# Kernel tuning notes

Hardware: AMD Instinct MI355X
Metric: run time of the kernel (lower is better)

The kernel has to match this reference:

```python
import jax, jax.numpy as jnp
import numpy as np

HID, EMB, VOCAB, NLAYERS = 512, 256, 64, 2
BS, SLEN, LLEN = 64, 128, 1024


def _p(key, shape, scale):
    return jax.random.normal(key, shape, dtype=jnp.float32) * scale


def setup_inputs() -> dict:
    key = jax.random.key(0)
    ks = jax.random.split(key, 24)
    s_h = 1.0 / np.sqrt(HID)
    inp = {
        "y": jax.random.randint(ks[0], (BS, SLEN), 0, VOCAB, dtype=jnp.int64),
        "encoder_h": jax.random.normal(ks[1], (BS, LLEN, HID), dtype=jnp.float32),
        # embedding table
        "emb": _p(ks[2], (VOCAB, EMB), 1.0),
        # attention LSTMCell: input = hidden + embedding
        "att_Wih": _p(ks[3], (4 * HID, HID + EMB), s_h),
        "att_Whh": _p(ks[4], (4 * HID, HID), s_h),
        "att_bih": _p(ks[5], (4 * HID,), s_h),
        "att_bhh": _p(ks[6], (4 * HID,), s_h),
        # stacked LSTMCells (NLAYERS, ...)
        "rnn_Wih": _p(ks[7], (NLAYERS, 4 * HID, HID), s_h),
        "rnn_Whh": _p(ks[8], (NLAYERS, 4 * HID, HID), s_h),
        "rnn_bih": _p(ks[9], (NLAYERS, 4 * HID), s_h),
        "rnn_bhh": _p(ks[10], (NLAYERS, 4 * HID), s_h),
        # AttentionContext mlp_s / mlp_h
        "Ws_w": _p(ks[11], (HID, HID), s_h),
        "Ws_b": _p(ks[12], (HID,), s_h),
        "Wh_w": _p(ks[13], (HID, HID), s_h),
        "Wh_b": _p(ks[14], (HID,), s_h),
        # output MLP: Linear(2H -> H), ReLU, Linear(H -> V)
        "W1": _p(ks[15], (HID, 2 * HID), 1.0 / np.sqrt(2 * HID)),
        "b1": _p(ks[16], (HID,), s_h),
        "W2": _p(ks[17], (VOCAB, HID), s_h),
        "b2": _p(ks[18], (VOCAB,), s_h),
    }
    return inp


def _lstm_cell(x, h, c, Wih, Whh, bih, bhh):
    gates = x @ Wih.T + bih + h @ Whh.T + bhh  # (B, 4H)
    i, f, g, o = jnp.split(gates, 4, axis=-1)
    c2 = jax.nn.sigmoid(f) * c + jax.nn.sigmoid(i) * jnp.tanh(g)
    h2 = jax.nn.sigmoid(o) * jnp.tanh(c2)
    return h2, c2


def reference(y, encoder_h, emb, att_Wih, att_Whh, att_bih, att_bhh,
              rnn_Wih, rnn_Whh, rnn_bih, rnn_bhh,
              Ws_w, Ws_b, Wh_w, Wh_b, W1, b1, W2, b2):
    B, S = y.shape
    H = att_Whh.shape[1]
    nl = rnn_Wih.shape[0]
    y_emb = emb[y]  # (B, S, E)
    # mlp_h(encoder_h) is loop-invariant; hoist it (same math as per-step recompute)
    h_e = encoder_h @ Wh_w.T + Wh_b  # (B, L, H)

    def step(carry, x_t):
        h0, c0, hs, cs, att = carry
        rnn_in = jnp.concatenate([x_t, att], axis=-1)  # (B, E+H)
        h0, c0 = _lstm_cell(rnn_in, h0, c0, att_Wih, att_Whh, att_bih, att_bhh)
        prev = h0
        new_h, new_c = [], []
        for l in range(nl):
            hl, cl = _lstm_cell(prev, hs[l], cs[l], rnn_Wih[l], rnn_Whh[l],
                                rnn_bih[l], rnn_bhh[l])
            new_h.append(hl)
            new_c.append(cl)
            prev = hl
        hs2 = jnp.stack(new_h)
        cs2 = jnp.stack(new_c)
        # attention on h_t[-1]
        s_e = prev @ Ws_w.T + Ws_b  # (B, H)
        e = jnp.einsum('bh,blh->bl', s_e, h_e)
        a = jax.nn.softmax(e, axis=-1)
        ctx = jnp.einsum('bl,blh->bh', a, h_e)  # (B, H)
        mlp_in = jnp.concatenate([prev, ctx], axis=-1)  # (B, 2H)
        logits = jax.nn.relu(mlp_in @ W1.T + b1) @ W2.T + b2  # (B, V)
        return (h0, c0, hs2, cs2, ctx), logits

    z = jnp.zeros((B, H), dtype=encoder_h.dtype)
    zz = jnp.zeros((nl, B, H), dtype=encoder_h.dtype)
    init = (z, z, zz, zz, z)
    _, y_out = jax.lax.scan(step, init, jnp.swapaxes(y_emb, 0, 1))  # (S, B, V)
    y_out = jnp.swapaxes(y_out, 0, 1)  # (B, S, V)
    return y_out.reshape(B * S, -1)
```

## Files before the change

### kernel.cpp

```cpp
#include <hip/hip_runtime.h>
#include <hip/hip_fp16.h>

#define HID   512
#define EMB   256
#define VOCAB 64
#define BS    64
#define SLEN  128
#define LLEN  1024
#define G4    2048
#define NB    256
#define NT    512
#define ASTR  66
#define ASZ   (128 * ASTR)

typedef unsigned u32x4 __attribute__((ext_vector_type(4)));

__device__ __forceinline__ u32x4 vldq(const unsigned* p) {
    return *reinterpret_cast<const volatile u32x4*>(p);
}
__device__ __forceinline__ float vld1(const float* p) {
    return *reinterpret_cast<const volatile float*>(p);
}
__device__ __forceinline__ void vst1(float* p, float v) {
    *reinterpret_cast<volatile float*>(p) = v;
}
__device__ __forceinline__ void vstu(unsigned* p, unsigned v) {
    *reinterpret_cast<volatile unsigned*>(p) = v;
}
__device__ __forceinline__ unsigned packh2(float x, float y) {
    __half2 h = __floats2half2_rn(x, y);
    return *reinterpret_cast<unsigned*>(&h);
}

struct SCell { float As[2 * ASZ]; float red[8][10][66]; };
struct SAttn { float u_s[512]; float w_s[32]; float msh[4];
               float accs[16][34]; unsigned enc[32 * 261]; };
struct SLog  { float red[16 * 33]; };
union SMem { SCell c; SAttn a; SLog lg; };

__device__ __forceinline__ void gridbar(unsigned* bar, unsigned nb)
{
    __syncthreads();
    const int t = threadIdx.x;
    if (t < 64) {
        if (t == 0)
            __hip_atomic_store(bar + blockIdx.x, nb, __ATOMIC_RELAXED,
                               __HIP_MEMORY_SCOPE_AGENT);
        for (;;) {
            bool ok = true;
#pragma unroll
            for (int i = 0; i < 4; ++i) {
                unsigned v = __hip_atomic_load(bar + i * 64 + t, __ATOMIC_RELAXED,
                                               __HIP_MEMORY_SCOPE_AGENT);
                ok &= (v >= nb);
            }
            if (__all((int)ok)) break;
            __builtin_amdgcn_s_sleep(1);
        }
    }
    __syncthreads();
}

__global__ __launch_bounds__(256)
void k_embed16T(const int* __restrict__ y, const float* __restrict__ emb,
                __half* __restrict__ xemb16)
{
    int i = blockIdx.x * 256 + threadIdx.x;
    int b  = i & 63;
    int e  = (i >> 6) & 255;
    int ts = i >> 14;
    xemb16[i] = __float2half(emb[y[b * SLEN + ts] * EMB + e]);
}

__global__ __launch_bounds__(256)
void k_cast(const float* __restrict__ src, __half* __restrict__ dst, int n4)
{
    int i = blockIdx.x * 256 + threadIdx.x;
    int stride = gridDim.x * 256;
    for (; i < n4; i += stride) {
        float4 v = reinterpret_cast<const float4*>(src)[i];
        reinterpret_cast<__half2*>(dst)[2 * i]     = __floats2half2_rn(v.x, v.y);
        reinterpret_cast<__half2*>(dst)[2 * i + 1] = __floats2half2_rn(v.z, v.w);
    }
}

__global__ __launch_bounds__(256)
void k_pmat(const float* __restrict__ Whw, const float* __restrict__ Wsw,
            const float* __restrict__ Wsb, float* __restrict__ P,
            float* __restrict__ p0)
{
    const int i = blockIdx.x;
    const int t = threadIdx.x;
    float a0 = 0.f, a1 = 0.f, ap = 0.f;
    for (int h = 0; h < HID; ++h) {
        float whi = Whw[h * HID + i];
        a0 += whi * Wsw[h * HID + t];
        a1 += whi * Wsw[h * HID + t + 256];
        ap += whi * Wsb[h];
    }
    P[i * HID + t]       = a0;
    P[i * HID + t + 256] = a1;
    if (t == 0) p0[i] = ap;
}

__global__ __launch_bounds__(256)
void k_fold(const float* __restrict__ aWih, const float* __restrict__ W1,
            const float* __restrict__ Whw, const float* __restrict__ Whb,
            const float* __restrict__ abih, const float* __restrict__ b1,
            float* __restrict__ Wp, float* __restrict__ W1bp,
            float* __restrict__ bihEff, float* __restrict__ b1eff)
{
    const int r = blockIdx.x;
    const int t = threadIdx.x;
    __shared__ float ssrc[512];
    const float* src;
    float* dst;
    if (r < G4) { src = aWih + (size_t)r * (EMB + HID) + EMB; dst = Wp + (size_t)r * HID; }
    else        { src = W1 + (size_t)(r - G4) * (2 * HID) + HID; dst = W1bp + (size_t)(r - G4) * HID; }
    ssrc[t]       = src[t];
    ssrc[t + 256] = src[t + 256];
    __syncthreads();
    float a0 = 0.f, a1 = 0.f;
    for (int h = 0; h < HID; ++h) {
        const float s = ssrc[h];
        a0 += s * Whw[h * HID + t];
        a1 += s * Whw[h * HID + t + 256];
    }
    dst[t]       = a0;
    dst[t + 256] = a1;
    if (t == 0) {
        float bb = 0.f;
        for (int h = 0; h < HID; ++h) bb += ssrc[h] * Whb[h];
        if (r < G4) bihEff[r] = abih[r] + bb;
        else        b1eff[r - G4] = b1[r - G4] + bb;
    }
}

template<int NTILES, int NR, bool VOL>
__device__ __forceinline__ void segScanT(float* As, const __half* A,
    const float* const* w, float* acc, int wv, int lane)
{
    const int t = threadIdx.x;
    const unsigned* ga = reinterpret_cast<const unsigned*>(A) + (size_t)t * 8;
    const int kRow = t >> 2;
    const int c0   = (t & 3) * 16;
    u32x4 Ra[2], Rb[2];

#define LOADT(R, j) do { const unsigned* _p = ga + (size_t)(j) * 4096;            \
        if (VOL) { R[0] = vldq(_p); R[1] = vldq(_p + 4); }                        \
        else { R[0] = *reinterpret_cast<const u32x4*>(_p);                        \
               R[1] = *reinterpret_cast<const u32x4*>(_p + 4); } } while (0)

    LOADT(Ra, 0);
    __syncthreads();
#pragma unroll
    for (int j = 0; j < NTILES; ++j) {
        float2* dst = reinterpret_cast<float2*>(As + (j & 1) * ASZ + kRow * ASTR + c0);
        const u32x4* R = (j & 1) ? Rb : Ra;
#pragma unroll
        for (int q = 0; q < 2; ++q)
#pragma unroll
            for (int h = 0; h < 4; ++h) {
                unsigned uw = R[q][h];
                dst[q * 4 + h] = __half22float2(*reinterpret_cast<const __half2*>(&uw));
            }
        if (j + 1 < NTILES) { if (j & 1) { LOADT(Ra, j + 1); } else { LOADT(Rb, j + 1); } }
        __syncthreads();
        const float* as = As + (j & 1) * ASZ + (wv * 16) * ASTR + lane;
#pragma unroll
        for (int kk = 0; kk < 16; ++kk) {
            const float a = as[kk * ASTR];
            const int k = j * 128 + wv * 16 + kk;
#pragma unroll
            for (int r = 0; r < NR; ++r)
                acc[r] += a * w[r][k];
        }
    }
#undef LOADT
}

__device__ __forceinline__ void packRows(__half* dstH, int i0, const float (&htmp)[2][64])
{
    const int t = threadIdx.x;
    if (t < 64) {
        const int hl = t >> 5;
        const int b2 = (t & 31) * 2;
        vstu(reinterpret_cast<unsigned*>(dstH) + (size_t)(i0 + hl) * 32 + (t & 31),
             packh2(htmp[hl][b2], htmp[hl][b2 + 1]));
    }
}

__device__ __forceinline__ void phaseA(SMem& sm, int i0,
    const __half* xT, const __half* chatT, const __half* h0rT,
    const float* __restrict__ aWih, const float* __restrict__ Wp,
    const float* __restrict__ aWhh, const float* __restrict__ W1bp,
    const float* __restrict__ bihEff, const float* __restrict__ abhh,
    float* cp, const float* hpartPriv, __half* h0wT, float* hid,
    float (&htmp)[2][64], int wv, int lane)
{
    float acc[10] = {};
    {
        const float* w8[8];
#pragma unroll
        for (int r = 0; r < 8; ++r)
            w8[r] = aWih + (size_t)((r >> 1) * HID + i0 + (r & 1)) * (EMB + HID);
        segScanT<2, 8, false>(sm.c.As, xT, w8, acc, wv, lane);
    }
    {
        const float* w10[10];
#pragma unroll
        for (int r = 0; r < 8; ++r)
            w10[r] = Wp + (size_t)((r >> 1) * HID + i0 + (r & 1)) * HID;
        w10[8] = W1bp + (size_t)i0 * HID;
        w10[9] = W1bp + (size_t)(i0 + 1) * HID;
        segScanT<4, 10, true>(sm.c.As, chatT, w10, acc, wv, lane);
    }
    {
        const float* w8[8];
#pragma unroll
        for (int r = 0; r < 8; ++r)
            w8[r] = aWhh + (size_t)((r >> 1) * HID + i0 + (r & 1)) * HID;
        segScanT<4, 8, true>(sm.c.As, h0rT, w8, acc, wv, lane);
    }
#pragma unroll
    for (int r = 0; r < 10; ++r) sm.c.red[wv][r][lane] = acc[r];
    __syncthreads();
    const int t = threadIdx.x;
    if (t < 128) {
        const int b = t & 63, hl = t >> 6;
        float gs[4];
#pragma unroll
        for (int g = 0; g < 4; ++g) {
            const int row = g * HID + i0 + hl;
            float s = bihEff[row] + abhh[row];
#pragma unroll
            for (int w = 0; w < 8; ++w) s += sm.c.red[w][g * 2 + hl][b];
            gs[g] = s;
        }
        const float ig = 1.f / (1.f + __expf(-gs[0]));
        const float fg = 1.f / (1.f + __expf(-gs[1]));
        const float gg = tanhf(gs[2]);
        const float og = 1.f / (1.f + __expf(-gs[3]));
        const float c2 = fg * cp[hl * 64 + b] + ig * gg;
        cp[hl * 64 + b] = c2;
        htmp[hl][b] = og * tanhf(c2);
    } else if (t < 256) {
        const int b = t & 63, hl = (t >> 6) - 2;
        float s = hpartPriv[hl * 64 + b];
#pragma unroll
        for (int w = 0; w < 8; ++w) s += sm.c.red[w][8 + hl][b];
        vst1(hid + (size_t)b * HID + i0 + hl, fmaxf(s, 0.f));
    }
    __syncthreads();
    packRows(h0wT, i0, htmp);
}

__device__ __forceinline__ void phaseR(SMem& sm, int i0,
    const __half* inT, const __half* recT,
    const float* __restrict__ Wih, const float* __restrict__ Whh,
    const float* __restrict__ bih, const float* __restrict__ bhh,
    float* cp, __half* hOutT, float (&htmp)[2][64], int wv, int lane)
{
    float acc[8] = {};
    {
        const float* w8[8];
#pragma unroll
        for (int r = 0; r < 8; ++r)
            w8[r] = Wih + (size_t)((r >> 1) * HID + i0 + (r & 1)) * HID;
        segScanT<4, 8, true>(sm.c.As, inT, w8, acc, wv, lane);
    }
    {
        const float* w8[8];
#pragma unroll
        for (int r = 0; r < 8; ++r)
            w8[r] = Whh + (size_t)((r >> 1) * HID + i0 + (r & 1)) * HID;
        segScanT<4, 8, true>(sm.c.As, recT, w8, acc, wv, lane);
    }
#pragma unroll
    for (int r = 0; r < 8; ++r) sm.c.red[wv][r][lane] = acc[r];
    __syncthreads();
    const int t = threadIdx.x;
    if (t < 128) {
        const int b = t & 63, hl = t >> 6;
        float gs[4];
#pragma unroll
        for (int g = 0; g < 4; ++g) {
            const int row = g * HID + i0 + hl;
            float s = bih[row] + bhh[row];
#pragma unroll
            for (int w = 0; w < 8; ++w) s += sm.c.red[w][g * 2 + hl][b];
            gs[g] = s;
        }
        const float ig = 1.f / (1.f + __expf(-gs[0]));
        const float fg = 1.f / (1.f + __expf(-gs[1]));
        const float gg = tanhf(gs[2]);
        const float og = 1.f / (1.f + __expf(-gs[3]));
        const float c2 = fg * cp[hl * 64 + b] + ig * gg;
        cp[hl * 64 + b] = c2;
        htmp[hl][b] = og * tanhf(c2);
    }
    __syncthreads();
    packRows(hOutT, i0, htmp);
}

__device__ __forceinline__ void logitsPhase(SMem& sm, int bid,
    const float* hid, const float* __restrict__ W2,
    const float* __restrict__ b2, float* __restrict__ out, int tstep)
{
    const int t  = threadIdx.x;
    const int b  = bid & 63;
    const int vg = bid >> 6;
    const int vp = t >> 5;
    const int kk = t & 31;
    float hreg[16];
    const float* hp = hid + (size_t)b * HID + kk * 16;
#pragma unroll
    for (int k = 0; k < 16; ++k) hreg[k] = vld1(hp + k);
    const float* w = W2 + (size_t)(vg * 16 + vp) * HID + kk * 16;
    float s = 0.f;
#pragma unroll
    for (int k = 0; k < 16; ++k) s += hreg[k] * w[k];
    __syncthreads();
    sm.lg.red[vp * 33 + kk] = s;
    __syncthreads();
    if (t < 16) {
        float acc = b2[vg * 16 + t];
#pragma unroll
        for (int k = 0; k < 32; ++k) acc += sm.lg.red[t * 33 + k];
        out[((size_t)b * SLEN + tstep) * VOCAB + vg * 16 + t] = acc;
    }
}

__device__ __forceinline__ void phaseD(SMem& sm, int i0,
    const __half* prevT, const float* __restrict__ Pm,
    const float* __restrict__ p0v, const float* __restrict__ W1,
    const float* __restrict__ b1eff, float* u, float* hpartPriv,
    int wv, int lane)
{
    float acc[4] = {};
    const float* w4[4];
    w4[0] = Pm + (size_t)i0 * HID;
    w4[1] = Pm + (size_t)(i0 + 1) * HID;
    w4[2] = W1 + (size_t)i0 * (2 * HID);
    w4[3] = W1 + (size_t)(i0 + 1) * (2 * HID);
    segScanT<4, 4, true>(sm.c.As, prevT, w4, acc, wv, lane);
#pragma unroll
    for (int r = 0; r < 4; ++r) sm.c.red[wv][r][lane] = acc[r];
    __syncthreads();
    const int t = threadIdx.x;
    if (t < 256) {
        const int b = t & 63, r = t >> 6;
        float s = 0.f;
#pragma unroll
        for (int w = 0; w < 8; ++w) s += sm.c.red[w][r][b];
        if (r < 2) vst1(u + (size_t)b * HID + i0 + r, s + p0v[i0 + r]);
        else       hpartPriv[(r - 2) * 64 + b] = s + b1eff[i0 + r - 2];
    }
}

__device__ __forceinline__ void phaseE(SMem& sm, int bid,
    const float* u, const __half* __restrict__ enc16,
    float* pm, float* ps, float* pv)
{
    const int t    = threadIdx.x;
    const int b    = bid >> 2;
    const int ch   = bid & 3;
    const int half = t >> 8;
    const int col  = t & 255;
    const int le   = t & 31;
    const int seg  = t >> 5;
    const int sq   = t & 15;
    const int sl   = (t >> 4) & 31;

    sm.a.u_s[t] = vld1(u + (size_t)b * HID + t);
    if (t == 0) { sm.a.msh[0] = -3.0e38f; sm.a.msh[1] = 0.f; sm.a.msh[2] = 0.f; }
    float vx = 0.f, vy = 0.f;

    const uint4* src = reinterpret_cast<const uint4*>(enc16 + ((size_t)b * LLEN + ch * 256) * HID);
    uint4 R[4];
#pragma unroll
    for (int p = 0; p < 4; ++p) R[p] = src[(size_t)sl * 64 + p * 16 + sq];
    __syncthreads();

    for (int blk = 0; blk < 8; ++blk) {
        {
            unsigned* dst = &sm.a.enc[sl * 261];
#pragma unroll
            for (int p = 0; p < 4; ++p) {
                const int c4 = (p * 16 + sq) * 4;
                dst[c4] = R[p].x; dst[c4+1] = R[p].y; dst[c4+2] = R[p].z; dst[c4+3] = R[p].w;
            }
        }
        __syncthreads();
        if (blk < 7) {
#pragma unroll
            for (int p = 0; p < 4; ++p)
                R[p] = src[((size_t)(blk + 1) * 32 + sl) * 64 + p * 16 + sq];
        }
        {
            float eacc = 0.f;
            const unsigned* er = &sm.a.enc[le * 261];
            const float* us = sm.a.u_s;
#pragma unroll
            for (int uu = 0; uu < 16; ++uu) {
                const int uo = seg * 16 + uu;
                unsigned uw = er[uo];
                float2 f2 = __half22float2(*reinterpret_cast<const __half2*>(&uw));
                eacc += us[2 * uo] * f2.x + us[2 * uo + 1] * f2.y;
            }
            sm.a.accs[seg][le] = eacc;
        }
        __syncthreads();
        if (t < 32) {
            float e = 0.f;
#pragma unroll
            for (int s2 = 0; s2 < 16; ++s2) e += sm.a.accs[s2][t];
            float bm = e;
#pragma unroll
            for (int off = 16; off > 0; off >>= 1) bm = fmaxf(bm, __shfl_xor(bm, off));
            const float m_old = sm.a.msh[0];
            const float m_new = fmaxf(m_old, bm);
            const float wl = __expf(e - m_new);
            float sw = wl;
#pragma unroll
            for (int off = 16; off > 0; off >>= 1) sw += __shfl_xor(sw, off);
            sm.a.w_s[t] = wl;
            if (t == 0) {
                const float sc = __expf(m_old - m_new);
                sm.a.msh[2] = sc;
                sm.a.msh[1] = sm.a.msh[1] * sc + sw;
                sm.a.msh[0] = m_new;
            }
        }
        __syncthreads();
        {
            const float sc = sm.a.msh[2];
            vx *= sc; vy *= sc;
#pragma unroll
            for (int ll = 0; ll < 16; ++ll) {
                const int l = half * 16 + ll;
                const float wl = sm.a.w_s[l];
                unsigned uw = sm.a.enc[l * 261 + col];
                float2 f2 = __half22float2(*reinterpret_cast<const __half2*>(&uw));
                vx += wl * f2.x; vy += wl * f2.y;
            }
        }
        __syncthreads();
    }
    if (half == 1) { sm.a.u_s[2 * col] = vx; sm.a.u_s[2 * col + 1] = vy; }
    __syncthreads();
    if (half == 0) {
        vx += sm.a.u_s[2 * col];
        vy += sm.a.u_s[2 * col + 1];
        const int pc = b * 4 + ch;
        vst1(pv + (size_t)pc * HID + 2 * col,     vx);
        vst1(pv + (size_t)pc * HID + 2 * col + 1, vy);
        if (t == 0) { vst1(pm + pc, sm.a.msh[0]); vst1(ps + pc, sm.a.msh[1]); }
    }
}

__device__ __forceinline__ void phaseF(int bid,
    const float* pm, const float* ps, const float* pv, __half* chatT)
{
    const int t = threadIdx.x;
    if (t < 128) {
        const int b = t & 63;
        const int j = bid * 2 + (t >> 6);
        float m[4], sd[4], pvv[4];
#pragma unroll
        for (int c = 0; c < 4; ++c) m[c]   = vld1(pm + b * 4 + c);
#pragma unroll
        for (int c = 0; c < 4; ++c) sd[c]  = vld1(ps + b * 4 + c);
#pragma unroll
        for (int c = 0; c < 4; ++c) pvv[c] = vld1(pv + (size_t)(b * 4 + c) * HID + j);
        float M = fmaxf(fmaxf(m[0], m[1]), fmaxf(m[2], m[3]));
        float den = 0.f, num = 0.f;
#pragma unroll
        for (int c = 0; c < 4; ++c) {
            float e = __expf(m[c] - M);
            den += e * sd[c]; num += e * pvv[c];
        }
        float v = num / den;
        float vn = __shfl_down(v, 1);
        if ((b & 1) == 0)
            vstu(reinterpret_cast<unsigned*>(chatT) + (size_t)j * 32 + (b >> 1),
                 packh2(v, vn));
    }
}

__device__ __forceinline__ void phaseT(SMem& sm, int i0,
    const __half* chatT, const float* __restrict__ W1bp,
    const float* hpartPriv, float* hid, int wv, int lane)
{
    float acc[2] = {};
    const float* w2[2];
    w2[0] = W1bp + (size_t)i0 * HID;
    w2[1] = W1bp + (size_t)(i0 + 1) * HID;
    segScanT<4, 2, true>(sm.c.As, chatT, w2, acc, wv, lane);
    sm.c.red[wv][0][lane] = acc[0];
    sm.c.red[wv][1][lane] = acc[1];
    __syncthreads();
    const int t = threadIdx.x;
    if (t < 128) {
        const int b = t & 63, r = t >> 6;
        float s = hpartPriv[r * 64 + b];
#pragma unroll
        for (int w = 0; w < 8; ++w) s += sm.c.red[w][r][b];
        vst1(hid + (size_t)b * HID + i0 + r, fmaxf(s, 0.f));
    }
}

__global__ __launch_bounds__(NT, 1)
void k_seq(const __half* __restrict__ xemb16, const __half* __restrict__ enc16,
           const float* __restrict__ aWih, const float* __restrict__ aWhh,
           const float* __restrict__ bihEff, const float* __restrict__ abhh,
           const float* __restrict__ rWih, const float* __restrict__ rWhh,
           const float* __restrict__ rbih, const float* __restrict__ rbhh,
           const float* __restrict__ Pm, const float* __restrict__ p0v,
           const float* __restrict__ W1, const float* __restrict__ b1eff,
           const float* __restrict__ Wp, const float* __restrict__ W1bp,
           const float* __restrict__ W2, const float* __restrict__ b2,
           __half* h0T, __half* hs0T, __half* hs1T, __half* chatT,
           float* u, float* hid, float* pv, float* pm, float* ps,
           float* out, unsigned* bar)
{
    __shared__ SMem sm;
    __shared__ float cPriv[3][128];
    __shared__ float hpartPriv[128];
    __shared__ float htmp[2][64];

    const int bid  = blockIdx.x;
    const int i0   = bid * 2;
    const int t0   = threadIdx.x;
    const int wv   = __builtin_amdgcn_readfirstlane(t0 >> 6);
    const int lane = t0 & 63;
    if (t0 < 128) { cPriv[0][t0] = 0.f; cPriv[1][t0] = 0.f; cPriv[2][t0] = 0.f;
                    hpartPriv[t0] = 0.f; }
    __syncthreads();

    unsigned nb = 0;
    for (int t = 0; t < SLEN; ++t) {
        const int par = t & 1;
        const __half* h0r  = h0T  + (size_t)par * 32768;
        __half*       h0w  = h0T  + (size_t)(par ^ 1) * 32768;
        const __half* hs0r = hs0T + (size_t)par * 32768;
        __half*       hs0w = hs0T + (size_t)(par ^ 1) * 32768;
        const __half* hs1r = hs1T + (size_t)par * 32768;
        __half*       hs1w = hs1T + (size_t)(par ^ 1) * 32768;

        phaseA(sm, i0, xemb16 + (size_t)t * BS * EMB, chatT, h0r,
               aWih, Wp, aWhh, W1bp, bihEff, abhh,
               cPriv[0], hpartPriv, h0w, hid, htmp, wv, lane);
        gridbar(bar, ++nb);
        phaseR(sm, i0, h0w, hs0r, rWih, rWhh, rbih, rbhh,
               cPriv[1], hs0w, htmp, wv, lane);
        gridbar(bar, ++nb);
        phaseR(sm, i0, hs0w, hs1r, rWih + (size_t)G4 * HID, rWhh + (size_t)G4 * HID,
               rbih + G4, rbhh + G4, cPriv[2], hs1w, htmp, wv, lane);
        gridbar(bar, ++nb);
        if (t > 0) logitsPhase(sm, bid, hid, W2, b2, out, t - 1);
        phaseD(sm, i0, hs1w, Pm, p0v, W1, b1eff, u, hpartPriv, wv, lane);
        gridbar(bar, ++nb);
        phaseE(sm, bid, u, enc16, pm, ps, pv);
        gridbar(bar, ++nb);
        phaseF(bid, pm, ps, pv, chatT);
        gridbar(bar, ++nb);
    }
    phaseT(sm, i0, chatT, W1bp, hpartPriv, hid, wv, lane);
    gridbar(bar, ++nb);
    logitsPhase(sm, bid, hid, W2, b2, out, SLEN - 1);
}

extern "C" void kernel_launch(void* const* d_in, const int* in_sizes, int n_in,
                              void* d_out, int out_size, void* d_ws, size_t ws_size,
                              hipStream_t stream)
{
    const int*   y    = (const int*)  d_in[0];
    const float* enc  = (const float*)d_in[1];
    const float* emb  = (const float*)d_in[2];
    const float* aWih = (const float*)d_in[3];
    const float* aWhh = (const float*)d_in[4];
    const float* abih = (const float*)d_in[5];
    const float* abhh = (const float*)d_in[6];
    const float* rWih = (const float*)d_in[7];
    const float* rWhh = (const float*)d_in[8];
    const float* rbih = (const float*)d_in[9];
    const float* rbhh = (const float*)d_in[10];
    const float* Wsw  = (const float*)d_in[11];
    const float* Wsb  = (const float*)d_in[12];
    const float* Whw  = (const float*)d_in[13];
    const float* Whb  = (const float*)d_in[14];
    const float* W1   = (const float*)d_in[15];
    const float* b1   = (const float*)d_in[16];
    const float* W2   = (const float*)d_in[17];
    const float* b2   = (const float*)d_in[18];
    float* out = (float*)d_out;

    char* base = (char*)d_ws;
    unsigned* bar = (unsigned*)base;                 base += 4096;
    __half* h0T   = (__half*)base;                   base += 2 * 65536;
    __half* hs0T  = (__half*)base;                   base += 2 * 65536;
    __half* hs1T  = (__half*)base;                   base += 2 * 65536;
    __half* chatT = (__half*)base;                   base += 65536;
    size_t zeroBytes = (size_t)(base - (char*)h0T);
    float* u      = (float*)base;                    base += 131072;
    float* hid    = (float*)base;                    base += 131072;
    float* pv     = (float*)base;                    base += 524288;
    float* pm     = (float*)base;                    base += 1024;
    float* ps     = (float*)base;                    base += 1024;
    float* Pm     = (float*)base;                    base += 1048576;
    float* p0v    = (float*)base;                    base += 2048;
    float* Wp     = (float*)base;                    base += (size_t)G4 * HID * 4;
    float* W1bp   = (float*)base;                    base += (size_t)HID * HID * 4;
    float* bihEff = (float*)base;                    base += 8192;
    float* b1eff  = (float*)base;                    base += 2048;
    __half* xemb16 = (__half*)base;                  base += (size_t)SLEN * BS * EMB * 2;
    __half* enc16  = (__half*)base;                  base += (size_t)BS * LLEN * HID * 2;
    size_t need = (size_t)(base - (char*)d_ws);
    if (ws_size < need) return;

    hipMemsetAsync(bar, 0, 4096, stream);
    hipMemsetAsync(h0T, 0, zeroBytes, stream);

    k_embed16T<<<(SLEN * BS * EMB) / 256, 256, 0, stream>>>(y, emb, xemb16);
    k_cast<<<4096, 256, 0, stream>>>(enc, enc16, (BS * LLEN * HID) / 4);
    k_pmat<<<HID, 256, 0, stream>>>(Whw, Wsw, Wsb, Pm, p0v);
    k_fold<<<G4 + HID, 256, 0, stream>>>(aWih, W1, Whw, Whb, abih, b1,
                                         Wp, W1bp, bihEff, b1eff);

    k_seq<<<NB, NT, 0, stream>>>(xemb16, enc16,
        aWih, aWhh, bihEff, abhh, rWih, rWhh, rbih, rbhh,
        Pm, p0v, W1, b1eff, Wp, W1bp, W2, b2,
        h0T, hs0T, hs1T, chatT, u, hid, pv, pm, ps, out, bar);
}
```

Measured before the change: 18.65 ms.

## Double block size to 1024 threads, splitting reductions across 16 waves

Raises the persistent kernel's threads per block from 512 to 1024 and re-partitions every phase to match. The LSTM segment scans now give each of 16 waves 8 K-rows instead of 16. The attention chunk splits its score and context reductions over twice as many lanes, and the logits phase splits K over 64 threads. The goal is more in-flight work per CU on the latency-bound sequential steps, at the cost of larger shared-memory reduction buffers, more reduction adds, and half the threads sitting idle during tile staging.

```diff
diff --git a/kernel.cpp b/kernel.cpp
--- a/kernel.cpp
+++ b/kernel.cpp
@@ -9,7 +9,8 @@
 #define LLEN  1024
 #define G4    2048
 #define NB    256
-#define NT    512
+#define NT    1024
+#define NW    16
 #define ASTR  66
 #define ASZ   (128 * ASTR)
 
@@ -32,10 +33,10 @@
     return *reinterpret_cast<unsigned*>(&h);
 }
 
-struct SCell { float As[2 * ASZ]; float red[8][10][66]; };
+struct SCell { float As[2 * ASZ]; float red[NW][10][66]; };
 struct SAttn { float u_s[512]; float w_s[32]; float msh[4];
-               float accs[16][34]; unsigned enc[32 * 261]; };
-struct SLog  { float red[16 * 33]; };
+               float accs[32][34]; float vred[4][512]; unsigned enc[32 * 261]; };
+struct SLog  { float red[16 * 65]; };
 union SMem { SCell c; SAttn a; SLog lg; };
 
 __device__ __forceinline__ void gridbar(unsigned* bar, unsigned nb)
@@ -141,8 +142,9 @@
     const float* const* w, float* acc, int wv, int lane)
 {
     const int t = threadIdx.x;
-    const unsigned* ga = reinterpret_cast<const unsigned*>(A) + (size_t)t * 8;
-    const int kRow = t >> 2;
+    const bool st = (t < 512);
+    const unsigned* ga = reinterpret_cast<const unsigned*>(A) + (size_t)(t & 511) * 8;
+    const int kRow = (t & 511) >> 2;
     const int c0   = (t & 3) * 16;
     u32x4 Ra[2], Rb[2];
 
@@ -151,26 +153,28 @@
         else { R[0] = *reinterpret_cast<const u32x4*>(_p);                        \
                R[1] = *reinterpret_cast<const u32x4*>(_p + 4); } } while (0)
 
-    LOADT(Ra, 0);
+    if (st) LOADT(Ra, 0);
     __syncthreads();
 #pragma unroll
     for (int j = 0; j < NTILES; ++j) {
-        float2* dst = reinterpret_cast<float2*>(As + (j & 1) * ASZ + kRow * ASTR + c0);
-        const u32x4* R = (j & 1) ? Rb : Ra;
-#pragma unroll
-        for (int q = 0; q < 2; ++q)
-#pragma unroll
-            for (int h = 0; h < 4; ++h) {
-                unsigned uw = R[q][h];
-                dst[q * 4 + h] = __half22float2(*reinterpret_cast<const __half2*>(&uw));
-            }
-        if (j + 1 < NTILES) { if (j & 1) { LOADT(Ra, j + 1); } else { LOADT(Rb, j + 1); } }
+        if (st) {
+            float2* dst = reinterpret_cast<float2*>(As + (j & 1) * ASZ + kRow * ASTR + c0);
+            const u32x4* R = (j & 1) ? Rb : Ra;
+#pragma unroll
+            for (int q = 0; q < 2; ++q)
+#pragma unroll
+                for (int h = 0; h < 4; ++h) {
+                    unsigned uw = R[q][h];
+                    dst[q * 4 + h] = __half22float2(*reinterpret_cast<const __half2*>(&uw));
+                }
+            if (j + 1 < NTILES) { if (j & 1) { LOADT(Ra, j + 1); } else { LOADT(Rb, j + 1); } }
+        }
         __syncthreads();
-        const float* as = As + (j & 1) * ASZ + (wv * 16) * ASTR + lane;
-#pragma unroll
-        for (int kk = 0; kk < 16; ++kk) {
+        const float* as = As + (j & 1) * ASZ + (wv * 8) * ASTR + lane;
+#pragma unroll
+        for (int kk = 0; kk < 8; ++kk) {
             const float a = as[kk * ASTR];
-            const int k = j * 128 + wv * 16 + kk;
+            const int k = j * 128 + wv * 8 + kk;
 #pragma unroll
             for (int r = 0; r < NR; ++r)
                 acc[r] += a * w[r][k];
@@ -234,7 +238,7 @@
             const int row = g * HID + i0 + hl;
             float s = bihEff[row] + abhh[row];
 #pragma unroll
-            for (int w = 0; w < 8; ++w) s += sm.c.red[w][g * 2 + hl][b];
+            for (int w = 0; w < NW; ++w) s += sm.c.red[w][g * 2 + hl][b];
             gs[g] = s;
         }
         const float ig = 1.f / (1.f + __expf(-gs[0]));
@@ -248,7 +252,7 @@
         const int b = t & 63, hl = (t >> 6) - 2;
         float s = hpartPriv[hl * 64 + b];
 #pragma unroll
-        for (int w = 0; w < 8; ++w) s += sm.c.red[w][8 + hl][b];
+        for (int w = 0; w < NW; ++w) s += sm.c.red[w][8 + hl][b];
         vst1(hid + (size_t)b * HID + i0 + hl, fmaxf(s, 0.f));
     }
     __syncthreads();
@@ -288,7 +292,7 @@
             const int row = g * HID + i0 + hl;
             float s = bih[row] + bhh[row];
 #pragma unroll
-            for (int w = 0; w < 8; ++w) s += sm.c.red[w][g * 2 + hl][b];
+            for (int w = 0; w < NW; ++w) s += sm.c.red[w][g * 2 + hl][b];
             gs[g] = s;
         }
         const float ig = 1.f / (1.f + __expf(-gs[0]));
@@ -310,23 +314,23 @@
     const int t  = threadIdx.x;
     const int b  = bid & 63;
     const int vg = bid >> 6;
-    const int vp = t >> 5;
-    const int kk = t & 31;
-    float hreg[16];
-    const float* hp = hid + (size_t)b * HID + kk * 16;
-#pragma unroll
-    for (int k = 0; k < 16; ++k) hreg[k] = vld1(hp + k);
-    const float* w = W2 + (size_t)(vg * 16 + vp) * HID + kk * 16;
+    const int vp = t >> 6;
+    const int kk = t & 63;
+    float hreg[8];
+    const float* hp = hid + (size_t)b * HID + kk * 8;
+#pragma unroll
+    for (int k = 0; k < 8; ++k) hreg[k] = vld1(hp + k);
+    const float* w = W2 + (size_t)(vg * 16 + vp) * HID + kk * 8;
     float s = 0.f;
 #pragma unroll
-    for (int k = 0; k < 16; ++k) s += hreg[k] * w[k];
-    __syncthreads();
-    sm.lg.red[vp * 33 + kk] = s;
+    for (int k = 0; k < 8; ++k) s += hreg[k] * w[k];
+    __syncthreads();
+    sm.lg.red[vp * 65 + kk] = s;
     __syncthreads();
     if (t < 16) {
         float acc = b2[vg * 16 + t];
 #pragma unroll
-        for (int k = 0; k < 32; ++k) acc += sm.lg.red[t * 33 + k];
+        for (int k = 0; k < 64; ++k) acc += sm.lg.red[t * 65 + k];
         out[((size_t)b * SLEN + tstep) * VOCAB + vg * 16 + t] = acc;
     }
 }
@@ -352,7 +356,7 @@
         const int b = t & 63, r = t >> 6;
         float s = 0.f;
 #pragma unroll
-        for (int w = 0; w < 8; ++w) s += sm.c.red[w][r][b];
+        for (int w = 0; w < NW; ++w) s += sm.c.red[w][r][b];
         if (r < 2) vst1(u + (size_t)b * HID + i0 + r, s + p0v[i0 + r]);
         else       hpartPriv[(r - 2) * 64 + b] = s + b1eff[i0 + r - 2];
     }
@@ -362,28 +366,30 @@
     const float* u, const __half* __restrict__ enc16,
     float* pm, float* ps, float* pv)
 {
-    const int t    = threadIdx.x;
-    const int b    = bid >> 2;
-    const int ch   = bid & 3;
-    const int half = t >> 8;
-    const int col  = t & 255;
-    const int le   = t & 31;
-    const int seg  = t >> 5;
-    const int sq   = t & 15;
-    const int sl   = (t >> 4) & 31;
-
-    sm.a.u_s[t] = vld1(u + (size_t)b * HID + t);
+    const int t   = threadIdx.x;
+    const int b   = bid >> 2;
+    const int ch  = bid & 3;
+    const int le  = t & 31;
+    const int seg = t >> 5;
+    const int sq  = t & 15;
+    const int sl  = (t >> 4) & 31;
+    const int rg  = t >> 8;
+    const int col = t & 255;
+
+    if (t < 512) sm.a.u_s[t] = vld1(u + (size_t)b * HID + t);
     if (t == 0) { sm.a.msh[0] = -3.0e38f; sm.a.msh[1] = 0.f; sm.a.msh[2] = 0.f; }
     float vx = 0.f, vy = 0.f;
 
     const uint4* src = reinterpret_cast<const uint4*>(enc16 + ((size_t)b * LLEN + ch * 256) * HID);
     uint4 R[4];
-#pragma unroll
-    for (int p = 0; p < 4; ++p) R[p] = src[(size_t)sl * 64 + p * 16 + sq];
+    if (t < 512) {
+#pragma unroll
+        for (int p = 0; p < 4; ++p) R[p] = src[(size_t)sl * 64 + p * 16 + sq];
+    }
     __syncthreads();
 
     for (int blk = 0; blk < 8; ++blk) {
-        {
+        if (t < 512) {
             unsigned* dst = &sm.a.enc[sl * 261];
 #pragma unroll
             for (int p = 0; p < 4; ++p) {
@@ -392,7 +398,7 @@
             }
         }
         __syncthreads();
-        if (blk < 7) {
+        if (t < 512 && blk < 7) {
 #pragma unroll
             for (int p = 0; p < 4; ++p)
                 R[p] = src[((size_t)(blk + 1) * 32 + sl) * 64 + p * 16 + sq];
@@ -402,8 +408,8 @@
             const unsigned* er = &sm.a.enc[le * 261];
             const float* us = sm.a.u_s;
 #pragma unroll
-            for (int uu = 0; uu < 16; ++uu) {
-                const int uo = seg * 16 + uu;
+            for (int uu = 0; uu < 8; ++uu) {
+                const int uo = seg * 8 + uu;
                 unsigned uw = er[uo];
                 float2 f2 = __half22float2(*reinterpret_cast<const __half2*>(&uw));
                 eacc += us[2 * uo] * f2.x + us[2 * uo + 1] * f2.y;
@@ -414,7 +420,7 @@
         if (t < 32) {
             float e = 0.f;
 #pragma unroll
-            for (int s2 = 0; s2 < 16; ++s2) e += sm.a.accs[s2][t];
+            for (int s2 = 0; s2 < 32; ++s2) e += sm.a.accs[s2][t];
             float bm = e;
 #pragma unroll
             for (int off = 16; off > 0; off >>= 1) bm = fmaxf(bm, __shfl_xor(bm, off));
@@ -437,8 +443,8 @@
             const float sc = sm.a.msh[2];
             vx *= sc; vy *= sc;
 #pragma unroll
-            for (int ll = 0; ll < 16; ++ll) {
-                const int l = half * 16 + ll;
+            for (int ll = 0; ll < 8; ++ll) {
+                const int l = rg * 8 + ll;
                 const float wl = sm.a.w_s[l];
                 unsigned uw = sm.a.enc[l * 261 + col];
                 float2 f2 = __half22float2(*reinterpret_cast<const __half2*>(&uw));
@@ -447,14 +453,13 @@
         }
         __syncthreads();
     }
-    if (half == 1) { sm.a.u_s[2 * col] = vx; sm.a.u_s[2 * col + 1] = vy; }
-    __syncthreads();
-    if (half == 0) {
-        vx += sm.a.u_s[2 * col];
-        vy += sm.a.u_s[2 * col + 1];
+    sm.a.vred[rg][2 * col]     = vx;
+    sm.a.vred[rg][2 * col + 1] = vy;
+    __syncthreads();
+    if (t < 512) {
+        float v = sm.a.vred[0][t] + sm.a.vred[1][t] + sm.a.vred[2][t] + sm.a.vred[3][t];
         const int pc = b * 4 + ch;
-        vst1(pv + (size_t)pc * HID + 2 * col,     vx);
-        vst1(pv + (size_t)pc * HID + 2 * col + 1, vy);
+        vst1(pv + (size_t)pc * HID + t, v);
         if (t == 0) { vst1(pm + pc, sm.a.msh[0]); vst1(ps + pc, sm.a.msh[1]); }
     }
 }
@@ -505,7 +510,7 @@
         const int b = t & 63, r = t >> 6;
         float s = hpartPriv[r * 64 + b];
 #pragma unroll
-        for (int w = 0; w < 8; ++w) s += sm.c.red[w][r][b];
+        for (int w = 0; w < NW; ++w) s += sm.c.red[w][r][b];
         vst1(hid + (size_t)b * HID + i0 + r, fmaxf(s, 0.f));
     }
 }
```

Result: faster. 17.71 ms (-5.1%).
